# Performance work log

Measured on AMD Instinct MI355X. Metric: run time of the kernel, lower is better.

The kernel has to match this reference:

```python
import jax, jax.numpy as jnp
import numpy as np

B, N, C = 32, 4096, 1152
TOPK_FRAC = 0.1


def setup_inputs() -> dict:
    key = jax.random.key(0)
    k1, k2 = jax.random.split(key)
    feature = jax.random.normal(k1, (B, N, C), dtype=jnp.float32)
    W = jax.random.normal(k2, (C,), dtype=jnp.float32) * 0.02  # conv1x1 weight [out=1, in=C, k=1] squeezed
    b = jnp.zeros((1,), dtype=jnp.float32)
    return {"feature": feature, "W": W, "b": b}


def reference(feature, W, b):
    # conv1x1 over [B, C, N] == per-patch dot product with W: [B, N]
    scores = jnp.einsum("bnc,c->bn", feature, W) + b[0]
    n = scores.shape[1]
    k = max(int(n * TOPK_FRAC), 1)  # static: 409
    topk_vals, _ = jax.lax.top_k(jnp.abs(scores), k)  # [B, k]
    per_sample = jnp.mean(topk_vals, axis=1)  # [B]
    # image_pyramid has a single level -> cat + mean over dim=1 is identity
    return [per_sample.reshape(-1, 1)]
```

## Files before the change

### kernel.cpp

```cpp
#include <hip/hip_runtime.h>

#define B_ 32
#define N_ 4096
#define C_ 1152
#define K_ 409

#define NBLK 2048
#define ITERS 16
#define SWEEP 8192

typedef float f32x4 __attribute__((ext_vector_type(4)));

__global__ __launch_bounds__(256) void score_abs_kernel(
    const float* __restrict__ feat, const float* __restrict__ W,
    const float* __restrict__ bias, float* __restrict__ absS) {
  __shared__ f32x4 Ws[C_ / 4];
  for (int i = threadIdx.x; i < C_ / 4; i += 256)
    Ws[i] = reinterpret_cast<const f32x4*>(W)[i];
  __syncthreads();

  const int wave = threadIdx.x >> 6;
  const int lane = threadIdx.x & 63;
  const float b0 = bias[0];

  const f32x4 w0 = Ws[lane];
  const f32x4 w1 = Ws[lane + 64];
  const f32x4 w2 = Ws[lane + 128];
  const f32x4 w3 = Ws[lane + 192];
  const f32x4 w4 = (lane < 32) ? Ws[256 + lane] : (f32x4)0.f;

  const int base = blockIdx.x * 4 + wave;
  const f32x4* fbase = reinterpret_cast<const f32x4*>(feat);
#pragma unroll 4
  for (int it = 0; it < ITERS; ++it) {
    const int patch = base + it * SWEEP;
    const f32x4* f4 = fbase + (size_t)patch * (C_ / 4);
    f32x4 vacc = __builtin_nontemporal_load(&f4[lane]) * w0;
    vacc += __builtin_nontemporal_load(&f4[lane + 64]) * w1;
    vacc += __builtin_nontemporal_load(&f4[lane + 128]) * w2;
    vacc += __builtin_nontemporal_load(&f4[lane + 192]) * w3;
    if (lane < 32) vacc += __builtin_nontemporal_load(&f4[256 + lane]) * w4;
    float acc = vacc[0] + vacc[1] + vacc[2] + vacc[3];
#pragma unroll
    for (int off = 32; off > 0; off >>= 1)
      acc += __shfl_down(acc, off, 64);
    if (lane == 0) absS[patch] = fabsf(acc + b0);
  }
}

__global__ __launch_bounds__(256) void topk_mean_kernel(
    const float* __restrict__ absS, float* __restrict__ out) {
  __shared__ float vals[N_];
  __shared__ unsigned hist[256];
  __shared__ unsigned wsum[4];
  __shared__ unsigned sel[2];
  __shared__ unsigned cred[4];
  __shared__ float sredf[4];

  const int t = threadIdx.x;
  const int wave = t >> 6;
  const int lane = t & 63;
  const int b = blockIdx.x;

  const float4* row4 = reinterpret_cast<const float4*>(absS + (size_t)b * N_);
  for (int i = t; i < N_ / 4; i += 256)
    reinterpret_cast<float4*>(vals)[i] = row4[i];
  __syncthreads();

  unsigned prefix = 0, k = K_;
#pragma unroll
  for (int p = 0; p < 4; ++p) {
    const int shift = 24 - 8 * p;
    const unsigned hmask = (p == 0) ? 0u : (0xFFFFFFFFu << (shift + 8));
    hist[t] = 0;
    __syncthreads();
    for (int i = t; i < N_; i += 256) {
      const unsigned e = __float_as_uint(vals[i]);
      if ((e & hmask) == (prefix & hmask))
        atomicAdd(&hist[(e >> shift) & 255u], 1u);
    }
    __syncthreads();
    const unsigned own = hist[t];
    unsigned x = own;
#pragma unroll
    for (int off = 1; off < 64; off <<= 1) {
      const unsigned v = __shfl_down(x, off, 64);
      if (lane + off < 64) x += v;
    }
    if (lane == 0) wsum[wave] = x;
    __syncthreads();
    unsigned cum_ge = x;
    for (int w = wave + 1; w < 4; ++w) cum_ge += wsum[w];
    const unsigned cnt_gt = cum_ge - own;
    if (cum_ge >= k && cnt_gt < k) {
      sel[0] = (unsigned)t;
      sel[1] = k - cnt_gt;
    }
    __syncthreads();
    prefix |= sel[0] << shift;
    k = sel[1];
    __syncthreads();
  }
  const float thr = __uint_as_float(prefix);

  float sum = 0.f;
  unsigned cgt = 0;
  for (int i = t; i < N_; i += 256) {
    const float v = vals[i];
    if (v > thr) { sum += v; cgt++; }
  }
#pragma unroll
  for (int off = 32; off > 0; off >>= 1) {
    sum += __shfl_down(sum, off, 64);
    cgt += __shfl_down(cgt, off, 64);
  }
  if (lane == 0) { cred[wave] = cgt; sredf[wave] = sum; }
  __syncthreads();
  if (t == 0) {
    const unsigned cg = cred[0] + cred[1] + cred[2] + cred[3];
    const float sg = sredf[0] + sredf[1] + sredf[2] + sredf[3];
    out[b] = (sg + (float)(K_ - (int)cg) * thr) / (float)K_;
  }
}

extern "C" void kernel_launch(void* const* d_in, const int* in_sizes, int n_in,
                              void* d_out, int out_size, void* d_ws, size_t ws_size,
                              hipStream_t stream) {
  const float* feat = (const float*)d_in[0];
  const float* W = (const float*)d_in[1];
  const float* bias = (const float*)d_in[2];
  float* out = (float*)d_out;
  float* absS = (float*)d_ws;

  score_abs_kernel<<<NBLK, 256, 0, stream>>>(feat, W, bias, absS);
  topk_mean_kernel<<<B_, 256, 0, stream>>>(absS, out);
}
```

Measured before the change: 111.7 us.

## Give each block contiguous patches, batch reductions, keep topk values in registers

```diff
diff --git a/kernel.cpp b/kernel.cpp
--- a/kernel.cpp
+++ b/kernel.cpp
@@ -6,8 +6,9 @@
 #define K_ 409
 
 #define NBLK 2048
-#define ITERS 16
-#define SWEEP 8192
+#define PATCH_PER_BLK 64
+#define GROUPS 4
+#define GITERS 4
 
 typedef float f32x4 __attribute__((ext_vector_type(4)));
 
@@ -29,28 +30,35 @@
   const f32x4 w3 = Ws[lane + 192];
   const f32x4 w4 = (lane < 32) ? Ws[256 + lane] : (f32x4)0.f;
 
-  const int base = blockIdx.x * 4 + wave;
+  const int patch_base = blockIdx.x * PATCH_PER_BLK + wave;
   const f32x4* fbase = reinterpret_cast<const f32x4*>(feat);
-#pragma unroll 4
-  for (int it = 0; it < ITERS; ++it) {
-    const int patch = base + it * SWEEP;
-    const f32x4* f4 = fbase + (size_t)patch * (C_ / 4);
-    f32x4 vacc = __builtin_nontemporal_load(&f4[lane]) * w0;
-    vacc += __builtin_nontemporal_load(&f4[lane + 64]) * w1;
-    vacc += __builtin_nontemporal_load(&f4[lane + 128]) * w2;
-    vacc += __builtin_nontemporal_load(&f4[lane + 192]) * w3;
-    if (lane < 32) vacc += __builtin_nontemporal_load(&f4[256 + lane]) * w4;
-    float acc = vacc[0] + vacc[1] + vacc[2] + vacc[3];
 #pragma unroll
-    for (int off = 32; off > 0; off >>= 1)
-      acc += __shfl_down(acc, off, 64);
-    if (lane == 0) absS[patch] = fabsf(acc + b0);
+  for (int g = 0; g < GROUPS; ++g) {
+    float pacc[GITERS];
+#pragma unroll
+    for (int u = 0; u < GITERS; ++u) {
+      const int patch = patch_base + (g * GITERS + u) * 4;
+      const f32x4* f4 = fbase + (size_t)patch * (C_ / 4);
+      f32x4 vacc = __builtin_nontemporal_load(&f4[lane]) * w0;
+      vacc += __builtin_nontemporal_load(&f4[lane + 64]) * w1;
+      vacc += __builtin_nontemporal_load(&f4[lane + 128]) * w2;
+      vacc += __builtin_nontemporal_load(&f4[lane + 192]) * w3;
+      if (lane < 32) vacc += __builtin_nontemporal_load(&f4[256 + lane]) * w4;
+      pacc[u] = vacc[0] + vacc[1] + vacc[2] + vacc[3];
+    }
+#pragma unroll
+    for (int u = 0; u < GITERS; ++u) {
+      float a = pacc[u];
+#pragma unroll
+      for (int off = 32; off > 0; off >>= 1) a += __shfl_down(a, off, 64);
+      if (lane == 0)
+        absS[patch_base + (g * GITERS + u) * 4] = fabsf(a + b0);
+    }
   }
 }
 
 __global__ __launch_bounds__(256) void topk_mean_kernel(
     const float* __restrict__ absS, float* __restrict__ out) {
-  __shared__ float vals[N_];
   __shared__ unsigned hist[256];
   __shared__ unsigned wsum[4];
   __shared__ unsigned sel[2];
@@ -60,12 +68,14 @@
   const int t = threadIdx.x;
   const int wave = t >> 6;
   const int lane = t & 63;
-  const int b = blockIdx.x;
+  const float4* row4 = reinterpret_cast<const float4*>(absS + (size_t)blockIdx.x * N_);
 
-  const float4* row4 = reinterpret_cast<const float4*>(absS + (size_t)b * N_);
-  for (int i = t; i < N_ / 4; i += 256)
-    reinterpret_cast<float4*>(vals)[i] = row4[i];
-  __syncthreads();
+  const float4 r0 = row4[t];
+  const float4 r1 = row4[t + 256];
+  const float4 r2 = row4[t + 512];
+  const float4 r3 = row4[t + 768];
+  float v[16] = {r0.x, r0.y, r0.z, r0.w, r1.x, r1.y, r1.z, r1.w,
+                 r2.x, r2.y, r2.z, r2.w, r3.x, r3.y, r3.z, r3.w};
 
   unsigned prefix = 0, k = K_;
 #pragma unroll
@@ -74,8 +84,9 @@
     const unsigned hmask = (p == 0) ? 0u : (0xFFFFFFFFu << (shift + 8));
     hist[t] = 0;
     __syncthreads();
-    for (int i = t; i < N_; i += 256) {
-      const unsigned e = __float_as_uint(vals[i]);
+#pragma unroll
+    for (int i = 0; i < 16; ++i) {
+      const unsigned e = __float_as_uint(v[i]);
       if ((e & hmask) == (prefix & hmask))
         atomicAdd(&hist[(e >> shift) & 255u], 1u);
     }
@@ -84,8 +95,8 @@
     unsigned x = own;
 #pragma unroll
     for (int off = 1; off < 64; off <<= 1) {
-      const unsigned v = __shfl_down(x, off, 64);
-      if (lane + off < 64) x += v;
+      const unsigned s = __shfl_down(x, off, 64);
+      if (lane + off < 64) x += s;
     }
     if (lane == 0) wsum[wave] = x;
     __syncthreads();
@@ -105,9 +116,9 @@
 
   float sum = 0.f;
   unsigned cgt = 0;
-  for (int i = t; i < N_; i += 256) {
-    const float v = vals[i];
-    if (v > thr) { sum += v; cgt++; }
+#pragma unroll
+  for (int i = 0; i < 16; ++i) {
+    if (v[i] > thr) { sum += v[i]; cgt++; }
   }
 #pragma unroll
   for (int off = 32; off > 0; off >>= 1) {
@@ -119,7 +130,7 @@
   if (t == 0) {
     const unsigned cg = cred[0] + cred[1] + cred[2] + cred[3];
     const float sg = sredf[0] + sredf[1] + sredf[2] + sredf[3];
-    out[b] = (sg + (float)(K_ - (int)cg) * thr) / (float)K_;
+    out[blockIdx.x] = (sg + (float)(K_ - (int)cg) * thr) / (float)K_;
   }
 }
 
```

Result: faster. 101.8 us (-8.9%).
